# Optimization experiments

Hardware: AMD Instinct MI355X
Metric: run time of the kernel (lower is better)

The kernel has to match this reference:

```python
import jax, jax.numpy as jnp
import numpy as np

C = 256          # channels
G = 4            # dcn groups
GC = C // G      # channels per group
K = 3            # dcn kernel size
P = K * K        # sampling points per group
OS = 0.5         # offset_scale
PAD = 1
N, H, W = 2, 128, 128


def setup_inputs() -> dict:
    key = jax.random.key(0)
    ks = jax.random.split(key, 8)
    f = lambda k, shp, s: jax.random.normal(k, shp, dtype=jnp.float32) * s
    return {
        "sampled_feat": jax.random.normal(ks[0], (N, H, W, C), dtype=jnp.float32),
        "context_info": jax.random.normal(ks[1], (N, H, W, C), dtype=jnp.float32),
        "W_in": f(ks[2], (C, C), 0.02),            # input_proj weight
        "b_in": jnp.zeros((C,), jnp.float32),
        "dw_kernel": f(ks[3], (3, 3, 1, C), 0.02),  # depthwise conv (HWIO, I=1)
        "dw_bias": jnp.zeros((C,), jnp.float32),
        "W_om": f(ks[4], (C, G * P * 3), 0.01),     # offset+mask projection
        "b_om": jnp.zeros((G * P * 3,), jnp.float32),
        "W_out": f(ks[5], (C, C), 0.02),            # output_proj (no bias)
        "ln_gamma": jnp.ones((C,), jnp.float32),
        "ln_beta": jnp.zeros((C,), jnp.float32),
    }


def _dcn_forward(sampled_feat, context_info, W_in, b_in, dw_kernel, dw_bias,
                 W_om, b_om, W_out, ln_gamma, ln_beta):
    Hp, Wp = H + 2 * PAD, W + 2 * PAD
    # value branch: pointwise input_proj then spatial zero-pad
    value = sampled_feat @ W_in + b_in
    value = jnp.pad(value, ((0, 0), (PAD, PAD), (PAD, PAD), (0, 0)))
    valg = value.reshape(N, Hp * Wp, G, GC).transpose(0, 2, 1, 3)  # (N,G,Hp*Wp,GC)

    # offset/mask branch (extra_offset_mask=True -> computed from context_info)
    ctx = jax.lax.conv_general_dilated(
        context_info, dw_kernel, (1, 1), ((1, 1), (1, 1)),
        dimension_numbers=("NHWC", "HWIO", "NHWC"), feature_group_count=C) + dw_bias
    om = (ctx @ W_om + b_om).reshape(N, H, W, G, 3 * P)
    offset = om[..., :2 * P].reshape(N, H, W, G, P, 2)  # (x,y) per sampling point
    mask = om[..., 2 * P:]                               # (N,H,W,G,P); DCNv4: no softmax

    # sampling locations in padded-input pixel coords (align_corners=False convention)
    kk = jnp.arange(K, dtype=jnp.float32) - (K - 1) // 2
    kx = jnp.tile(kk, K)      # (P,)
    ky = jnp.repeat(kk, K)    # (P,)
    base_x = (jnp.arange(W, dtype=jnp.float32) + PAD)[None, None, :, None, None]
    base_y = (jnp.arange(H, dtype=jnp.float32) + PAD)[None, :, None, None, None]
    px = base_x + OS * (kx + offset[..., 0])   # (N,H,W,G,P)
    py = base_y + OS * (ky + offset[..., 1])
    px = px.transpose(0, 3, 1, 2, 4).reshape(N, G, -1)  # (N,G,H*W*P)
    py = py.transpose(0, 3, 1, 2, 4).reshape(N, G, -1)

    # bilinear sampling with zero padding outside the padded input
    x0 = jnp.floor(px); y0 = jnp.floor(py)
    wx1 = px - x0; wy1 = py - y0

    def corner(xi, yi, w):
        valid = (xi >= 0) & (xi <= Wp - 1) & (yi >= 0) & (yi <= Hp - 1)
        idx = (jnp.clip(yi, 0, Hp - 1) * Wp + jnp.clip(xi, 0, Wp - 1)).astype(jnp.int32)
        v = jnp.take_along_axis(valg, idx[..., None], axis=2)  # (N,G,S,GC)
        return v * (w * valid)[..., None]

    samp = (corner(x0, y0, (1 - wx1) * (1 - wy1))
            + corner(x0 + 1, y0, wx1 * (1 - wy1))
            + corner(x0, y0 + 1, (1 - wx1) * wy1)
            + corner(x0 + 1, y0 + 1, wx1 * wy1))
    samp = samp.reshape(N, G, H, W, P, GC)
    maskg = mask.transpose(0, 3, 1, 2, 4)  # (N,G,H,W,P)
    out = jnp.einsum("nghwpc,nghwp->nhwgc", samp, maskg).reshape(N, H, W, C)

    out = out @ W_out  # output_proj, output_bias=False
    # LayerNorm over channels + exact GELU
    mu = out.mean(-1, keepdims=True)
    var = out.var(-1, keepdims=True)
    out = (out - mu) * jax.lax.rsqrt(var + 1e-5) * ln_gamma + ln_beta
    return jax.nn.gelu(out, approximate=False)


def reference(sampled_feat, context_info, W_in, b_in, dw_kernel, dw_bias,
              W_om, b_om, W_out, ln_gamma, ln_beta):
    return _dcn_forward(sampled_feat, context_info, W_in, b_in, dw_kernel, dw_bias,
                        W_om, b_om, W_out, ln_gamma, ln_beta)
```

## Files before the change

kernel.cpp:

```cpp
#include <hip/hip_runtime.h>
#include <math.h>

constexpr int NBATCH = 2, HH = 128, WW = 128, CC = 256;
constexpr int PP = 9, OMW = 108;
constexpr int MM = NBATCH * HH * WW;
constexpr int BTCOLS = 640;

using bf8 = __attribute__((ext_vector_type(8))) short;
using f32x4 = __attribute__((ext_vector_type(4))) float;

__device__ __forceinline__ short f2bf(float x) {
  unsigned u = __builtin_bit_cast(unsigned, x);
  unsigned r = (u + 0x7fffu + ((u >> 16) & 1u)) >> 16;
  return (short)r;
}
__device__ __forceinline__ float bf2f(short h) {
  unsigned u = ((unsigned)(unsigned short)h) << 16;
  return __builtin_bit_cast(float, u);
}
__device__ __forceinline__ unsigned pack_hi16(float x, float y) {
  return __builtin_amdgcn_perm(__builtin_bit_cast(unsigned, y),
                               __builtin_bit_cast(unsigned, x), 0x07060302u);
}
__device__ __forceinline__ float trunc_hi(float x) {
  return __builtin_bit_cast(float, __builtin_bit_cast(unsigned, x) & 0xFFFF0000u);
}

__global__ __launch_bounds__(256) void prep_kernel(
    const float* __restrict__ Win, const float* __restrict__ Wom,
    const float* __restrict__ Wout, short* __restrict__ Bh,
    short* __restrict__ Bl) {
  int gid = blockIdx.x * 256 + threadIdx.x;
  int col = gid >> 8, k = gid & 255;
  float w;
  if (col < 256)
    w = Win[k * 256 + col];
  else if (col < 384) {
    int c = col - 256;
    w = (c < OMW) ? Wom[k * OMW + c] : 0.f;
  } else {
    int c = col - 384;
    w = Wout[k * 256 + c];
  }
  short h = f2bf(w);
  Bh[gid] = h;
  Bl[gid] = f2bf(w - bf2f(h));
}

__global__ __launch_bounds__(256) void dwconv_kernel(
    const float* __restrict__ x, const float* __restrict__ k,
    const float* __restrict__ b, float* __restrict__ y) {
  int gid = blockIdx.x * 256 + threadIdx.x;
  int q = gid & 63;
  int m = gid >> 6;
  int c = q * 4;
  int w = m & 127, h = (m >> 7) & 127, n = m >> 14;
  float4 acc = *(const float4*)&b[c];
#pragma unroll
  for (int dy = 0; dy < 3; ++dy) {
    int yy = h + dy - 1;
    if (yy < 0 || yy >= HH) continue;
#pragma unroll
    for (int dx = 0; dx < 3; ++dx) {
      int xx = w + dx - 1;
      if (xx < 0 || xx >= WW) continue;
      float4 v = *(const float4*)&x[(((size_t)n * HH + yy) * WW + xx) * CC + c];
      float4 kk = *(const float4*)&k[(dy * 3 + dx) * CC + c];
      acc.x += v.x * kk.x;
      acc.y += v.y * kk.y;
      acc.z += v.z * kk.z;
      acc.w += v.w * kk.w;
    }
  }
  *(float4*)&y[(size_t)m * CC + c] = acc;
}

template <bool GUARD, bool BIAS>
__global__ __launch_bounds__(256, 3) void mgemm(
    const float* __restrict__ Af, const short* __restrict__ Bth,
    const short* __restrict__ Btl, const float* __restrict__ bias,
    float* __restrict__ Co, int nshift, int nout) {
  constexpr int BM = 64, BN = 128, BK = 64, SK = 68;
  __shared__ __align__(16) short As[2][BM * SK];
  __shared__ __align__(16) short Bs[2][BN * SK];
  const int t = threadIdx.x;
  const int lane = t & 63, wid = t >> 6;
  const int wr = wid >> 1, wc = wid & 1;
  const int l15 = lane & 15, l4 = lane >> 4;
  const int mb = ((int)blockIdx.x >> nshift) * BM;
  const int nb = ((int)blockIdx.x & ((1 << nshift) - 1)) * BN;

  f32x4 acc[2][4];
#pragma unroll
  for (int r = 0; r < 2; ++r)
#pragma unroll
    for (int n = 0; n < 4; ++n) acc[r][n] = (f32x4){0.f, 0.f, 0.f, 0.f};

  for (int ks = 0; ks < 256; ks += BK) {
#pragma unroll
    for (int i = 0; i < 4; ++i) {
      int idx = t + 256 * i;
      int row = idx >> 4, kq = (idx & 15) * 4;
      float4 v = *(const float4*)&Af[(size_t)(mb + row) * 256 + ks + kq];
      unsigned h01 = pack_hi16(v.x, v.y);
      unsigned h23 = pack_hi16(v.z, v.w);
      unsigned l01 = pack_hi16(v.x - trunc_hi(v.x), v.y - trunc_hi(v.y));
      unsigned l23 = pack_hi16(v.z - trunc_hi(v.z), v.w - trunc_hi(v.w));
      uint2 hw, lw;
      hw.x = h01; hw.y = h23; lw.x = l01; lw.y = l23;
      *(uint2*)&As[0][row * SK + kq] = hw;
      *(uint2*)&As[1][row * SK + kq] = lw;
    }
#pragma unroll
    for (int i = 0; i < 4; ++i) {
      int idx = t + 256 * i;
      int col = idx >> 3, kq = (idx & 7) * 8;
      size_t g = (size_t)(nb + col) * 256 + ks + kq;
      *(bf8*)&Bs[0][col * SK + kq] = *(const bf8*)&Bth[g];
      *(bf8*)&Bs[1][col * SK + kq] = *(const bf8*)&Btl[g];
    }
    __syncthreads();
#pragma unroll
    for (int kk = 0; kk < 2; ++kk) {
      int ko = kk * 32 + l4 * 8;
      bf8 ah[2], al[2], bh[4], bl[4];
#pragma unroll
      for (int r = 0; r < 2; ++r) {
        int row = wr * 32 + r * 16 + l15;
        ah[r] = *(const bf8*)&As[0][row * SK + ko];
        al[r] = *(const bf8*)&As[1][row * SK + ko];
      }
#pragma unroll
      for (int n = 0; n < 4; ++n) {
        int col = wc * 64 + n * 16 + l15;
        bh[n] = *(const bf8*)&Bs[0][col * SK + ko];
        bl[n] = *(const bf8*)&Bs[1][col * SK + ko];
      }
#pragma unroll
      for (int r = 0; r < 2; ++r)
#pragma unroll
        for (int n = 0; n < 4; ++n) {
          acc[r][n] = __builtin_amdgcn_mfma_f32_16x16x32_bf16(al[r], bh[n],
                                                              acc[r][n], 0, 0, 0);
          acc[r][n] = __builtin_amdgcn_mfma_f32_16x16x32_bf16(ah[r], bl[n],
                                                              acc[r][n], 0, 0, 0);
          acc[r][n] = __builtin_amdgcn_mfma_f32_16x16x32_bf16(ah[r], bh[n],
                                                              acc[r][n], 0, 0, 0);
        }
    }
    __syncthreads();
  }

#pragma unroll
  for (int r = 0; r < 2; ++r)
#pragma unroll
    for (int reg = 0; reg < 4; ++reg) {
      int row = mb + wr * 32 + r * 16 + l4 * 4 + reg;
#pragma unroll
      for (int n = 0; n < 4; ++n) {
        int col = nb + wc * 64 + n * 16 + l15;
        if (!GUARD || col < nout) {
          float v = acc[r][n][reg];
          if constexpr (BIAS) v += bias[col];
          Co[(size_t)row * nout + col] = v;
        }
      }
    }
}

__global__ __launch_bounds__(256) void sample_kernel(
    const float* __restrict__ val, const float* __restrict__ om,
    float* __restrict__ outp) {
  __shared__ float wwin[4][4][12];
  __shared__ int fflag[4][4];
  const int t = threadIdx.x;
  const int m0 = (int)blockIdx.x * 4;

  if (t < 192) ((float*)wwin)[t] = 0.f;
  if (t < 16) ((int*)fflag)[t] = 0;
  __syncthreads();

  if (t < 144) {
    int pix = t / 36, r = t % 36;
    int g = r / 9, p = r % 9;
    int m = m0 + pix;
    int w = m & 127, h = (m >> 7) & 127;
    const float* omp = om + (size_t)m * OMW + g * 27;
    float ox = omp[2 * p], oy = omp[2 * p + 1], mk = omp[18 + p];
    float px = (float)(w + 1) + 0.5f * ((float)(p % 3 - 1) + ox);
    float py = (float)(h + 1) + 0.5f * ((float)(p / 3 - 1) + oy);
    float x0f = floorf(px), y0f = floorf(py);
    int x0 = (int)x0f, y0 = (int)y0f;
    float wx1 = px - x0f, wy1 = py - y0f;
    float wx0 = 1.f - wx1, wy0 = 1.f - wy1;
#pragma unroll
    for (int j = 0; j < 2; ++j)
#pragma unroll
      for (int i = 0; i < 2; ++i) {
        int cx = x0 + i, cy = y0 + j;
        if (cx < 1 || cx > 128 || cy < 1 || cy > 128) continue;
        float cw = mk * (i ? wx1 : wx0) * (j ? wy1 : wy0);
        int rx = cx - w, ry = cy - h;
        if ((unsigned)rx > 2u || (unsigned)ry > 2u)
          atomicOr(&fflag[pix][g], 1);
        else
          atomicAdd(&wwin[pix][g][ry * 3 + rx], cw);
      }
  }
  __syncthreads();

  const int pix = t >> 6, g = (t >> 4) & 3, cq = t & 15;
  const int q = g * 16 + cq;
  const int m = m0 + pix;
  const int w = m & 127, h = (m >> 7) & 127, n = m >> 14;
  const float* vb = val + ((size_t)n << 22) + (q << 2);
  float4 acc = make_float4(0.f, 0.f, 0.f, 0.f);

  if (fflag[pix][g] == 0) {
#pragma unroll
    for (int ry = 0; ry < 3; ++ry)
#pragma unroll
      for (int rx = 0; rx < 3; ++rx) {
        float cw = wwin[pix][g][ry * 3 + rx];
        int xi = min(max(w - 1 + rx, 0), 127);
        int yi = min(max(h - 1 + ry, 0), 127);
        float4 v = *(const float4*)&vb[((yi << 7) + xi) << 8];
        acc.x += cw * v.x;
        acc.y += cw * v.y;
        acc.z += cw * v.z;
        acc.w += cw * v.w;
      }
  } else {
    const float* omp = om + (size_t)m * OMW + g * 27;
    float bx = (float)(w + 1), by = (float)(h + 1);
#pragma unroll
    for (int p = 0; p < PP; ++p) {
      float px = bx + 0.5f * ((float)(p % 3 - 1) + omp[2 * p]);
      float py = by + 0.5f * ((float)(p / 3 - 1) + omp[2 * p + 1]);
      float mk = omp[18 + p];
      float x0f = floorf(px), y0f = floorf(py);
      int x0 = (int)x0f, y0 = (int)y0f;
      float wx1 = px - x0f, wy1 = py - y0f;
      float wx0 = 1.f - wx1, wy0 = 1.f - wy1;
      float4 s = make_float4(0.f, 0.f, 0.f, 0.f);
#define CORNER(XC, YC, WT)                                            \
  {                                                                   \
    int xc = (XC), yc = (YC);                                         \
    int xi = min(max(xc, 1), 128), yi = min(max(yc, 1), 128);         \
    float wt = ((xc == xi) && (yc == yi)) ? (WT) : 0.f;               \
    const float4 v =                                                  \
        *(const float4*)&vb[(((yi - 1) << 7) + (xi - 1)) << 8];       \
    s.x += v.x * wt;                                                  \
    s.y += v.y * wt;                                                  \
    s.z += v.z * wt;                                                  \
    s.w += v.w * wt;                                                  \
  }
      CORNER(x0, y0, wx0 * wy0);
      CORNER(x0 + 1, y0, wx1 * wy0);
      CORNER(x0, y0 + 1, wx0 * wy1);
      CORNER(x0 + 1, y0 + 1, wx1 * wy1);
#undef CORNER
      acc.x += mk * s.x;
      acc.y += mk * s.y;
      acc.z += mk * s.z;
      acc.w += mk * s.w;
    }
  }
  *(float4*)&outp[((size_t)m << 8) + (q << 2)] = acc;
}

__global__ __launch_bounds__(256) void ln_gelu_kernel(
    const float* __restrict__ x, const float* __restrict__ gam,
    const float* __restrict__ bet, float* __restrict__ y) {
  int row = blockIdx.x * 4 + (threadIdx.x >> 6);
  int lane = threadIdx.x & 63;
  const float* xr = x + (size_t)row * 256 + lane * 4;
  float4 v = *(const float4*)xr;
  float s = v.x + v.y + v.z + v.w;
  float ss = v.x * v.x + v.y * v.y + v.z * v.z + v.w * v.w;
#pragma unroll
  for (int m = 1; m < 64; m <<= 1) {
    s += __shfl_xor(s, m);
    ss += __shfl_xor(ss, m);
  }
  float mu = s * (1.f / 256.f);
  float var = ss * (1.f / 256.f) - mu * mu;
  float rs = rsqrtf(var + 1e-5f);
  float4 gg = *(const float4*)&gam[lane * 4];
  float4 bb = *(const float4*)&bet[lane * 4];
  float4 o;
#define GEL(FIELD)                                                   \
  {                                                                  \
    float t_ = (v.FIELD - mu) * rs * gg.FIELD + bb.FIELD;            \
    o.FIELD = 0.5f * t_ * (1.f + erff(t_ * 0.70710678118654752f));   \
  }
  GEL(x) GEL(y) GEL(z) GEL(w)
#undef GEL
  *(float4*)&y[(size_t)row * 256 + lane * 4] = o;
}

extern "C" void kernel_launch(void* const* d_in, const int* in_sizes, int n_in,
                              void* d_out, int out_size, void* d_ws,
                              size_t ws_size, hipStream_t stream) {
  (void)in_sizes;
  (void)n_in;
  (void)out_size;
  (void)ws_size;
  const float* sampled = (const float*)d_in[0];
  const float* ctxin = (const float*)d_in[1];
  const float* W_in = (const float*)d_in[2];
  const float* b_in = (const float*)d_in[3];
  const float* dwk = (const float*)d_in[4];
  const float* dwb = (const float*)d_in[5];
  const float* W_om = (const float*)d_in[6];
  const float* b_om = (const float*)d_in[7];
  const float* W_out = (const float*)d_in[8];
  const float* lng = (const float*)d_in[9];
  const float* lnb = (const float*)d_in[10];
  float* out = (float*)d_out;

  float* value = (float*)d_ws;
  float* omb = value + (size_t)MM * CC;
  float* ctx = omb + (size_t)MM * OMW;
  short* Bth = (short*)(ctx + (size_t)MM * CC);
  short* Btl = Bth + (size_t)BTCOLS * 256;
  float* dcn = ctx;
  float* out_pre = value;

  prep_kernel<<<BTCOLS, 256, 0, stream>>>(W_in, W_om, W_out, Bth, Btl);
  dwconv_kernel<<<MM * 64 / 256, 256, 0, stream>>>(ctxin, dwk, dwb, ctx);
  mgemm<true, true><<<MM / 64, 256, 0, stream>>>(ctx, Bth + 256 * 256,
                                                 Btl + 256 * 256, b_om, omb, 0,
                                                 OMW);
  mgemm<false, true><<<2 * (MM / 64), 256, 0, stream>>>(sampled, Bth, Btl,
                                                        b_in, value, 1, 256);
  sample_kernel<<<MM / 4, 256, 0, stream>>>(value, omb, dcn);
  mgemm<false, false><<<2 * (MM / 64), 256, 0, stream>>>(
      dcn, Bth + 384 * 256, Btl + 384 * 256, nullptr, out_pre, 1, 256);
  ln_gelu_kernel<<<MM / 4, 256, 0, stream>>>(out_pre, lng, lnb, out);
}
```

Before: 239.2 us.

## Fuse LayerNorm+GELU into output GEMM epilogue and template GEMM tile sizes

Templates the split-bf16 MFMA GEMM on tile sizes and warp layout. It gives the input projection a 128x128 tile and makes the output projection cover full 256-column rows, so LayerNorm statistics and exact GELU can be computed in the epilogue. The separate ln_gelu kernel and its extra round trip of the pre-norm tensor through global memory are removed. The trade-off is larger register and LDS use, with occupancy lowered to 2 blocks per unit, and less parallelism in the final GEMM.

New measurement: 230.4 us. 3.7% less time.

```diff
diff --git a/kernel.cpp b/kernel.cpp
--- a/kernel.cpp
+++ b/kernel.cpp
@@ -75,71 +75,73 @@
   *(float4*)&y[(size_t)m * CC + c] = acc;
 }
 
-template <bool GUARD, bool BIAS>
-__global__ __launch_bounds__(256, 3) void mgemm(
+template <int BM, int BN, int BK, int WM, int WN, bool GUARD, bool BIAS,
+          bool LN>
+__global__ __launch_bounds__(256, 2) void mgemm(
     const float* __restrict__ Af, const short* __restrict__ Bth,
     const short* __restrict__ Btl, const float* __restrict__ bias,
-    float* __restrict__ Co, int nshift, int nout) {
-  constexpr int BM = 64, BN = 128, BK = 64, SK = 68;
+    float* __restrict__ Co, const float* __restrict__ lng,
+    const float* __restrict__ lnb, int nshift, int nout) {
+  constexpr int SK = BK + 4;
+  constexpr int R = BM / (16 * WM), C = BN / (16 * WN);
   __shared__ __align__(16) short As[2][BM * SK];
   __shared__ __align__(16) short Bs[2][BN * SK];
   const int t = threadIdx.x;
   const int lane = t & 63, wid = t >> 6;
-  const int wr = wid >> 1, wc = wid & 1;
+  const int wr = wid / WN, wc = wid % WN;
   const int l15 = lane & 15, l4 = lane >> 4;
   const int mb = ((int)blockIdx.x >> nshift) * BM;
   const int nb = ((int)blockIdx.x & ((1 << nshift) - 1)) * BN;
 
-  f32x4 acc[2][4];
-#pragma unroll
-  for (int r = 0; r < 2; ++r)
-#pragma unroll
-    for (int n = 0; n < 4; ++n) acc[r][n] = (f32x4){0.f, 0.f, 0.f, 0.f};
+  f32x4 acc[R][C];
+#pragma unroll
+  for (int r = 0; r < R; ++r)
+#pragma unroll
+    for (int n = 0; n < C; ++n) acc[r][n] = (f32x4){0.f, 0.f, 0.f, 0.f};
 
   for (int ks = 0; ks < 256; ks += BK) {
 #pragma unroll
-    for (int i = 0; i < 4; ++i) {
+    for (int i = 0; i < BM * BK / 4 / 256; ++i) {
       int idx = t + 256 * i;
-      int row = idx >> 4, kq = (idx & 15) * 4;
+      int row = idx / (BK / 4), kq = (idx % (BK / 4)) * 4;
       float4 v = *(const float4*)&Af[(size_t)(mb + row) * 256 + ks + kq];
-      unsigned h01 = pack_hi16(v.x, v.y);
-      unsigned h23 = pack_hi16(v.z, v.w);
-      unsigned l01 = pack_hi16(v.x - trunc_hi(v.x), v.y - trunc_hi(v.y));
-      unsigned l23 = pack_hi16(v.z - trunc_hi(v.z), v.w - trunc_hi(v.w));
       uint2 hw, lw;
-      hw.x = h01; hw.y = h23; lw.x = l01; lw.y = l23;
+      hw.x = pack_hi16(v.x, v.y);
+      hw.y = pack_hi16(v.z, v.w);
+      lw.x = pack_hi16(v.x - trunc_hi(v.x), v.y - trunc_hi(v.y));
+      lw.y = pack_hi16(v.z - trunc_hi(v.z), v.w - trunc_hi(v.w));
       *(uint2*)&As[0][row * SK + kq] = hw;
       *(uint2*)&As[1][row * SK + kq] = lw;
     }
 #pragma unroll
-    for (int i = 0; i < 4; ++i) {
+    for (int i = 0; i < BN * BK / 8 / 256; ++i) {
       int idx = t + 256 * i;
-      int col = idx >> 3, kq = (idx & 7) * 8;
+      int col = idx / (BK / 8), kq = (idx % (BK / 8)) * 8;
       size_t g = (size_t)(nb + col) * 256 + ks + kq;
       *(bf8*)&Bs[0][col * SK + kq] = *(const bf8*)&Bth[g];
       *(bf8*)&Bs[1][col * SK + kq] = *(const bf8*)&Btl[g];
     }
     __syncthreads();
 #pragma unroll
-    for (int kk = 0; kk < 2; ++kk) {
+    for (int kk = 0; kk < BK / 32; ++kk) {
       int ko = kk * 32 + l4 * 8;
-      bf8 ah[2], al[2], bh[4], bl[4];
-#pragma unroll
-      for (int r = 0; r < 2; ++r) {
-        int row = wr * 32 + r * 16 + l15;
+      bf8 ah[R], al[R], bh[C], bl[C];
+#pragma unroll
+      for (int r = 0; r < R; ++r) {
+        int row = (wr * R + r) * 16 + l15;
         ah[r] = *(const bf8*)&As[0][row * SK + ko];
         al[r] = *(const bf8*)&As[1][row * SK + ko];
       }
 #pragma unroll
-      for (int n = 0; n < 4; ++n) {
-        int col = wc * 64 + n * 16 + l15;
+      for (int n = 0; n < C; ++n) {
+        int col = (wc * C + n) * 16 + l15;
         bh[n] = *(const bf8*)&Bs[0][col * SK + ko];
         bl[n] = *(const bf8*)&Bs[1][col * SK + ko];
       }
 #pragma unroll
-      for (int r = 0; r < 2; ++r)
-#pragma unroll
-        for (int n = 0; n < 4; ++n) {
+      for (int r = 0; r < R; ++r)
+#pragma unroll
+        for (int n = 0; n < C; ++n) {
           acc[r][n] = __builtin_amdgcn_mfma_f32_16x16x32_bf16(al[r], bh[n],
                                                               acc[r][n], 0, 0, 0);
           acc[r][n] = __builtin_amdgcn_mfma_f32_16x16x32_bf16(ah[r], bl[n],
@@ -151,21 +153,78 @@
     __syncthreads();
   }
 
-#pragma unroll
-  for (int r = 0; r < 2; ++r)
-#pragma unroll
-    for (int reg = 0; reg < 4; ++reg) {
-      int row = mb + wr * 32 + r * 16 + l4 * 4 + reg;
-#pragma unroll
-      for (int n = 0; n < 4; ++n) {
-        int col = nb + wc * 64 + n * 16 + l15;
-        if (!GUARD || col < nout) {
+  if constexpr (LN) {
+    static_assert(WM == 1 && BM == 64, "LN layout");
+    __shared__ float red_s[64][WN], red_ss[64][WN];
+    __shared__ float mu_s[64], rs_s[64];
+#pragma unroll
+    for (int r = 0; r < R; ++r)
+#pragma unroll
+      for (int reg = 0; reg < 4; ++reg) {
+        float s = 0.f, ss = 0.f;
+#pragma unroll
+        for (int n = 0; n < C; ++n) {
           float v = acc[r][n][reg];
-          if constexpr (BIAS) v += bias[col];
-          Co[(size_t)row * nout + col] = v;
-        }
-      }
-    }
+          s += v;
+          ss += v * v;
+        }
+#pragma unroll
+        for (int mk = 1; mk < 16; mk <<= 1) {
+          s += __shfl_xor(s, mk);
+          ss += __shfl_xor(ss, mk);
+        }
+        if (l15 == 0) {
+          int row = r * 16 + l4 * 4 + reg;
+          red_s[row][wc] = s;
+          red_ss[row][wc] = ss;
+        }
+      }
+    __syncthreads();
+    if (t < 64) {
+      float s = 0.f, ss = 0.f;
+#pragma unroll
+      for (int p = 0; p < WN; ++p) {
+        s += red_s[t][p];
+        ss += red_ss[t][p];
+      }
+      float mu = s * (1.f / 256.f);
+      float var = ss * (1.f / 256.f) - mu * mu;
+      mu_s[t] = mu;
+      rs_s[t] = rsqrtf(var + 1e-5f);
+    }
+    __syncthreads();
+#pragma unroll
+    for (int r = 0; r < R; ++r)
+#pragma unroll
+      for (int reg = 0; reg < 4; ++reg) {
+        int rloc = r * 16 + l4 * 4 + reg;
+        int row = mb + rloc;
+        float mu = mu_s[rloc], rs = rs_s[rloc];
+#pragma unroll
+        for (int n = 0; n < C; ++n) {
+          int col = (wc * C + n) * 16 + l15;
+          float v = (acc[r][n][reg] - mu) * rs * lng[col] + lnb[col];
+          Co[(size_t)row * 256 + col] =
+              0.5f * v * (1.f + erff(v * 0.70710678118654752f));
+        }
+      }
+  } else {
+#pragma unroll
+    for (int r = 0; r < R; ++r)
+#pragma unroll
+      for (int reg = 0; reg < 4; ++reg) {
+        int row = mb + (wr * R + r) * 16 + l4 * 4 + reg;
+#pragma unroll
+        for (int n = 0; n < C; ++n) {
+          int col = nb + (wc * C + n) * 16 + l15;
+          if (!GUARD || col < nout) {
+            float v = acc[r][n][reg];
+            if constexpr (BIAS) v += bias[col];
+            Co[(size_t)row * nout + col] = v;
+          }
+        }
+      }
+  }
 }
 
 __global__ __launch_bounds__(256) void sample_kernel(
@@ -269,36 +328,6 @@
   *(float4*)&outp[((size_t)m << 8) + (q << 2)] = acc;
 }
 
-__global__ __launch_bounds__(256) void ln_gelu_kernel(
-    const float* __restrict__ x, const float* __restrict__ gam,
-    const float* __restrict__ bet, float* __restrict__ y) {
-  int row = blockIdx.x * 4 + (threadIdx.x >> 6);
-  int lane = threadIdx.x & 63;
-  const float* xr = x + (size_t)row * 256 + lane * 4;
-  float4 v = *(const float4*)xr;
-  float s = v.x + v.y + v.z + v.w;
-  float ss = v.x * v.x + v.y * v.y + v.z * v.z + v.w * v.w;
-#pragma unroll
-  for (int m = 1; m < 64; m <<= 1) {
-    s += __shfl_xor(s, m);
-    ss += __shfl_xor(ss, m);
-  }
-  float mu = s * (1.f / 256.f);
-  float var = ss * (1.f / 256.f) - mu * mu;
-  float rs = rsqrtf(var + 1e-5f);
-  float4 gg = *(const float4*)&gam[lane * 4];
-  float4 bb = *(const float4*)&bet[lane * 4];
-  float4 o;
-#define GEL(FIELD)                                                   \
-  {                                                                  \
-    float t_ = (v.FIELD - mu) * rs * gg.FIELD + bb.FIELD;            \
-    o.FIELD = 0.5f * t_ * (1.f + erff(t_ * 0.70710678118654752f));   \
-  }
-  GEL(x) GEL(y) GEL(z) GEL(w)
-#undef GEL
-  *(float4*)&y[(size_t)row * 256 + lane * 4] = o;
-}
-
 extern "C" void kernel_launch(void* const* d_in, const int* in_sizes, int n_in,
                               void* d_out, int out_size, void* d_ws,
                               size_t ws_size, hipStream_t stream) {
@@ -325,17 +354,16 @@
   short* Bth = (short*)(ctx + (size_t)MM * CC);
   short* Btl = Bth + (size_t)BTCOLS * 256;
   float* dcn = ctx;
-  float* out_pre = value;
 
   prep_kernel<<<BTCOLS, 256, 0, stream>>>(W_in, W_om, W_out, Bth, Btl);
   dwconv_kernel<<<MM * 64 / 256, 256, 0, stream>>>(ctxin, dwk, dwb, ctx);
-  mgemm<true, true><<<MM / 64, 256, 0, stream>>>(ctx, Bth + 256 * 256,
-                                                 Btl + 256 * 256, b_om, omb, 0,
-                                                 OMW);
-  mgemm<false, true><<<2 * (MM / 64), 256, 0, stream>>>(sampled, Bth, Btl,
-                                                        b_in, value, 1, 256);
+  mgemm<64, 128, 64, 2, 2, true, true, false><<<MM / 64, 256, 0, stream>>>(
+      ctx, Bth + 256 * 256, Btl + 256 * 256, b_om, omb, nullptr, nullptr, 0,
+      OMW);
+  mgemm<128, 128, 64, 2, 2, false, true, false>
+      <<<2 * (MM / 128), 256, 0, stream>>>(sampled, Bth, Btl, b_in, value,
+                                           nullptr, nullptr, 1, 256);
   sample_kernel<<<MM / 4, 256, 0, stream>>>(value, omb, dcn);
-  mgemm<false, false><<<2 * (MM / 64), 256, 0, stream>>>(
-      dcn, Bth + 384 * 256, Btl + 384 * 256, nullptr, out_pre, 1, 256);
-  ln_gelu_kernel<<<MM / 4, 256, 0, stream>>>(out_pre, lng, lnb, out);
-}
+  mgemm<64, 256, 32, 1, 4, false, false, true><<<MM / 64, 256, 0, stream>>>(
+      dcn, Bth + 384 * 256, Btl + 384 * 256, nullptr, out, lng, lnb, 0, 256);
+}
```
